# Optimization experiments

Hardware: AMD Instinct MI355X
Metric: run time of the kernel (lower is better)

## Reference

```python
import jax, jax.numpy as jnp
import numpy as np

B, S, V, E, H, XD, C = 64, 512, 32000, 512, 1024, 512, 1024


def setup_inputs() -> dict:
    key = jax.random.key(0)
    ks = jax.random.split(key, 20)
    s = 0.02
    inp = {
        "X": jax.random.randint(ks[0], (B, S), 0, V),
        "h0": jax.random.normal(ks[1], (B, H), jnp.float32),
        "embed": jax.random.normal(ks[2], (V, E), jnp.float32) * s,
        "Wzh": jax.random.normal(ks[3], (H, H), jnp.float32) * s,
        "bzh": jnp.zeros((H,), jnp.float32),
        "Wzx": jax.random.normal(ks[4], (H, E), jnp.float32) * s,
        "bzx": jnp.zeros((H,), jnp.float32),
        "Wrh": jax.random.normal(ks[5], (H, H), jnp.float32) * s,
        "brh": jnp.zeros((H,), jnp.float32),
        "Wrx": jax.random.normal(ks[6], (H, E), jnp.float32) * s,
        "brx": jnp.zeros((H,), jnp.float32),
        "Wuh": jax.random.normal(ks[7], (H, H), jnp.float32) * s,
        "buh": jnp.zeros((H,), jnp.float32),
        "Wux": jax.random.normal(ks[8], (H, E), jnp.float32) * s,
        "bux": jnp.zeros((H,), jnp.float32),
        "Wxh": jax.random.normal(ks[9], (XD, H), jnp.float32) * s,
        "bxh": jnp.zeros((XD,), jnp.float32),
        "Wc": jax.random.normal(ks[10], (C, XD), jnp.float32) * s,
        "bc": jnp.zeros((C,), jnp.float32),
    }
    return inp


def reference(X, h0, embed, Wzh, bzh, Wzx, bzx, Wrh, brh, Wrx, brx,
              Wuh, buh, Wux, bux, Wxh, bxh, Wc, bc):
    x_embed = embed[X]                    # [B,S,E]
    xs = jnp.transpose(x_embed, (1, 0, 2))  # [S,B,E] for scan

    def step(ht, xt):
        zt = jax.nn.sigmoid(ht @ Wzh.T + bzh + xt @ Wzx.T + bzx)
        rt = jax.nn.sigmoid(ht @ Wrh.T + brh + xt @ Wrx.T + brx)
        ht_cand = jnp.tanh((rt * ht) @ Wuh.T + buh + xt @ Wux.T + bux)
        ht_new = (1.0 - zt) * ht + zt * ht_cand
        yt = ht_new @ Wxh.T + bxh          # [B,XD]
        yprob = yt @ Wc.T + bc             # [B,C]
        return ht_new, yprob

    _, yprobs = jax.lax.scan(step, h0, xs)  # [S,B,C]
    return jnp.transpose(yprobs, (1, 0, 2))  # [B,S,C]
```

## Files before the change

### kernel.cpp

```cpp
#include <hip/hip_runtime.h>

#define DEV __device__ __forceinline__

using bf16x8 = __attribute__((ext_vector_type(8))) short;
using u16x4  = __attribute__((ext_vector_type(4))) unsigned short;
using f32x4  = __attribute__((ext_vector_type(4))) float;

constexpr int B_ = 64, S_ = 512, V_ = 32000, E_ = 512, H_ = 1024, C_ = 1024;
constexpr int NWG = 64;
constexpr int JS  = 16;

constexpr size_t OFF_FH    = 0;
constexpr size_t OFF_FR    = 1024;
constexpr size_t OFF_BIASG = 2048;
constexpr size_t OFF_BCOMB = OFF_BIASG + 3072*4;
constexpr size_t OFF_HB    = OFF_BCOMB + 1024*4;
constexpr size_t OFF_RHB   = OFF_HB + 131072;
constexpr size_t OFF_WCOMB = OFF_RHB + 131072;
constexpr size_t OFF_WXALL = OFF_WCOMB + (size_t)C_*H_*2;
constexpr size_t OFF_WZF   = OFF_WXALL + (size_t)3072*512*2;
constexpr size_t OFF_WRF   = OFF_WZF + (size_t)NWG*32768;
constexpr size_t OFF_WUF   = OFF_WRF + (size_t)NWG*32768;
constexpr size_t OFF_EMB   = OFF_WUF + (size_t)NWG*32768;
constexpr size_t OFF_G     = OFF_EMB + (size_t)V_*E_*2;
constexpr size_t OFF_HS    = OFF_G + (size_t)S_*B_*3072*2;
constexpr size_t WS_NEED   = OFF_HS + (size_t)S_*B_*H_*2;

DEV unsigned short f2bf(float f){
  unsigned int x; __builtin_memcpy(&x, &f, 4);
  x += 0x7fffu + ((x>>16)&1u);
  return (unsigned short)(x>>16);
}
DEV float bf2f(unsigned short u){
  unsigned int x = ((unsigned int)u)<<16; float f; __builtin_memcpy(&f,&x,4); return f;
}

DEV int4 ld16_coh(const char* p){
  int4 r;
  asm volatile("global_load_dwordx4 %0, %1, off sc0 sc1" : "=v"(r) : "v"(p) : "memory");
  return r;
}
DEV void st16_coh(char* p, bf16x8 v){
  asm volatile("global_store_dwordx4 %0, %1, off sc0 sc1" :: "v"(p), "v"(v) : "memory");
}
DEV uint2 ld8_plain(const char* p){
  uint2 r;
  asm volatile("global_load_dwordx2 %0, %1, off" : "=v"(r) : "v"(p) : "memory");
  return r;
}

#define WAITVM(N) do{ asm volatile("s_waitcnt vmcnt(" #N ")" ::: "memory"); \
                      __builtin_amdgcn_sched_barrier(0); }while(0)
#define WAITLGKM() do{ asm volatile("s_waitcnt lgkmcnt(0)" ::: "memory"); \
                       __builtin_amdgcn_sched_barrier(0); }while(0)

__global__ void k_cvt_embed(const float* __restrict__ src, unsigned short* __restrict__ dst){
  for (int i = blockIdx.x*blockDim.x + threadIdx.x; i < V_*E_; i += gridDim.x*blockDim.x)
    dst[i] = f2bf(src[i]);
}

__global__ void k_build_wx(const float* __restrict__ Wzx, const float* __restrict__ Wrx,
                           const float* __restrict__ Wux, unsigned short* __restrict__ out){
  for (int i = blockIdx.x*blockDim.x + threadIdx.x; i < 3072*512; i += gridDim.x*blockDim.x){
    int n = i>>9, k = i&511;
    int g = n>>10, r = n&1023;
    const float* W = (g==0) ? Wzx : (g==1) ? Wrx : Wux;
    out[i] = f2bf(W[(size_t)r*512 + k]);
  }
}

__global__ void k_biasg(const float* bzh, const float* bzx, const float* brh, const float* brx,
                        const float* buh, const float* bux, float* __restrict__ out){
  for (int i = blockIdx.x*blockDim.x + threadIdx.x; i < 3072; i += gridDim.x*blockDim.x){
    int g = i>>10, r = i&1023;
    float v = (g==0) ? (bzh[r]+bzx[r]) : (g==1) ? (brh[r]+brx[r]) : (buh[r]+bux[r]);
    out[i] = v;
  }
}

__global__ void k_fragW(const float* __restrict__ W, unsigned short* __restrict__ out){
  for (int i = blockIdx.x*blockDim.x + threadIdx.x; i < NWG*32*64*8; i += gridDim.x*blockDim.x){
    int e=i&7, l=(i>>3)&63, ck=(i>>9)&31, g=i>>14;
    out[i] = f2bf(W[(size_t)(g*JS+(l&15))*H_ + ck*32 + ((l>>4)<<3) + e]);
  }
}

__global__ __launch_bounds__(256) void k_wcomb(const float* __restrict__ Wc,
                                               const float* __restrict__ Wxh,
                                               unsigned short* __restrict__ Wcomb){
  __shared__ float wc[16][512];
  const int c0 = blockIdx.x*16;
  const int tid = threadIdx.x;
  for (int q = tid; q < 16*512; q += 256)
    wc[q>>9][q&511] = Wc[(size_t)(c0 + (q>>9))*512 + (q&511)];
  __syncthreads();
  const int h4 = tid*4;
  f32x4 acc[16];
  #pragma unroll
  for (int ci=0; ci<16; ++ci) acc[ci] = (f32x4){0.f,0.f,0.f,0.f};
  for (int x=0; x<512; ++x){
    f32x4 wv = *(const f32x4*)(Wxh + (size_t)x*H_ + h4);
    #pragma unroll
    for (int ci=0; ci<16; ++ci) acc[ci] += wc[ci][x] * wv;
  }
  #pragma unroll
  for (int ci=0; ci<16; ++ci)
    #pragma unroll
    for (int e=0; e<4; ++e)
      Wcomb[(size_t)(c0+ci)*H_ + h4 + e] = f2bf(acc[ci][e]);
}

__global__ void k_bcomb(const float* __restrict__ Wc, const float* __restrict__ bxh,
                        const float* __restrict__ bc, float* __restrict__ out){
  int c = blockIdx.x*blockDim.x + threadIdx.x;
  if (c >= C_) return;
  float s = bc[c];
  for (int x=0; x<512; ++x) s += Wc[(size_t)c*512 + x]*bxh[x];
  out[c] = s;
}

__global__ void k_hinit(const float* __restrict__ h0, unsigned short* __restrict__ hbF){
  int i = blockIdx.x*256 + threadIdx.x;
  int e=i&7, l=(i>>3)&63, ck=(i>>9)&31, q=i>>14;
  hbF[i] = f2bf(h0[(size_t)(q*16+(l&15))*H_ + ck*32 + ((l>>4)<<3) + e]);
}

template<bool GATHER, int MODE>
__global__ __launch_bounds__(256) void gemm_bt(
  const unsigned short* __restrict__ Asrc, const int* __restrict__ Xidx,
  const unsigned short* __restrict__ embB,
  const unsigned short* __restrict__ Bw, const float* __restrict__ bias,
  void* __restrict__ Cout, int K, int KT, int NTN, int ldc)
{
  __shared__ unsigned short ldsA[128*64];
  __shared__ unsigned short ldsB[128*64];
  const int bid = blockIdx.x;
  const int tm = bid / NTN, tn = bid % NTN;
  const int m0 = tm*128, n0 = tn*128;
  const int tid = threadIdx.x, wave = tid>>6, lane = tid&63;
  const int wm = (wave&1)*64, wn = (wave>>1)*64;

  const char* srcA[4]; const char* srcB[4];
  int rr[4], cc[4];
  #pragma unroll
  for (int s=0; s<4; ++s){
    int L = s*4096 + tid*16;
    int r = L>>7, cb = L&127;
    rr[s]=r; cc[s]=cb;
    if constexpr (GATHER){
      int m = m0 + r; int tt = m>>6, bb = m&63;
      srcA[s] = (const char*)(embB + (size_t)Xidx[bb*S_ + tt]*(size_t)K);
    } else {
      srcA[s] = (const char*)(Asrc + (size_t)(m0+r)*(size_t)K);
    }
    srcB[s] = (const char*)(Bw + (size_t)(n0+r)*(size_t)K);
  }

  f32x4 acc[4][4];
  #pragma unroll
  for (int a=0;a<4;a++)
    #pragma unroll
    for (int b=0;b<4;b++) acc[a][b] = (f32x4){0.f,0.f,0.f,0.f};

  int4 ra[4], rb[4];
  auto loadRegs = [&](int kt){
    #pragma unroll
    for (int s=0;s<4;s++){
      ra[s] = *(const int4*)(srcA[s] + (size_t)kt*128 + cc[s]);
      rb[s] = *(const int4*)(srcB[s] + (size_t)kt*128 + cc[s]);
    }
  };
  auto writeLDS = [&](){
    #pragma unroll
    for (int s=0;s<4;s++){
      int off = (rr[s]<<7) + (cc[s] ^ ((rr[s]&7)<<4));
      *(int4*)((char*)ldsA + off) = ra[s];
      *(int4*)((char*)ldsB + off) = rb[s];
    }
  };

  loadRegs(0);
  for (int kt=0; kt<KT; ++kt){
    __syncthreads();
    writeLDS();
    if (kt+1 < KT) loadRegs(kt+1);
    __syncthreads();
    #pragma unroll
    for (int ck=0; ck<2; ++ck){
      bf16x8 af[4], bfr[4];
      #pragma unroll
      for (int q=0;q<4;q++){
        int ar = wm + q*16 + (lane&15);
        int ao = (ar<<7) + (((ck<<6) + ((lane>>4)<<4)) ^ ((ar&7)<<4));
        af[q] = *(const bf16x8*)((const char*)ldsA + ao);
        int br = wn + q*16 + (lane&15);
        int bo = (br<<7) + (((ck<<6) + ((lane>>4)<<4)) ^ ((br&7)<<4));
        bfr[q] = *(const bf16x8*)((const char*)ldsB + bo);
      }
      #pragma unroll
      for (int mi=0;mi<4;mi++)
        #pragma unroll
        for (int ni=0;ni<4;ni++)
          acc[mi][ni] = __builtin_amdgcn_mfma_f32_16x16x32_bf16(af[mi], bfr[ni], acc[mi][ni], 0,0,0);
    }
  }

  #pragma unroll
  for (int mi=0;mi<4;mi++){
    #pragma unroll
    for (int ni=0;ni<4;ni++){
      int gm = m0 + wm + mi*16 + ((lane>>4)<<2);
      int gn = n0 + wn + ni*16 + (lane&15);
      float bv = bias[gn];
      if constexpr (MODE == 1){
        #pragma unroll
        for (int r2=0;r2<4;r2++){
          float v = acc[mi][ni][r2] + bv;
          int m = gm + r2;
          ((float*)Cout)[ (size_t)((m&63)*S_ + (m>>6))*(size_t)ldc + gn ] = v;
        }
      } else {
        int t0 = gm>>6, b0 = gm&63;
        u16x4 pk;
        #pragma unroll
        for (int r2=0;r2<4;r2++) pk[r2] = f2bf(acc[mi][ni][r2] + bv);
        *(u16x4*)((unsigned short*)Cout + ((size_t)t0*3072 + gn)*64 + b0) = pk;
      }
    }
  }
}

DEV void pollq(const unsigned int* f, unsigned int p, int lane, int bg){
  const unsigned int* a = f + lane*4 + bg;
  int guard = 0;
  for(;;){
    unsigned int v = __hip_atomic_load(a, __ATOMIC_RELAXED, __HIP_MEMORY_SCOPE_AGENT);
    if (__all((int)(v >= p))) break;
    __builtin_amdgcn_s_sleep(1);
    if (++guard > (1<<24)) break;
  }
}

__global__ __launch_bounds__(256,1) void k_scan(const float* __restrict__ h0, char* __restrict__ ws){
  const int wg = blockIdx.x;
  const int tid = threadIdx.x;
  const int bg = tid>>6, lane = tid&63;
  const int j0 = wg*JS;
  const int ckw = wg>>1, hw = wg&1;

  unsigned int* fH = (unsigned int*)(ws + OFF_FH);
  unsigned int* fR = (unsigned int*)(ws + OFF_FR);
  const unsigned short* G = (const unsigned short*)(ws + OFF_G);
  unsigned short* Hs  = (unsigned short*)(ws + OFF_HS);

  const char* EXH = ws + OFF_HB  + ((size_t)bg<<15);
  const char* EXR = ws + OFF_RHB + ((size_t)bg<<15);
  char* pubR = ws + OFF_RHB + ((size_t)bg<<15) + (ckw<<10) + (hw<<9);
  char* pubH = ws + OFF_HB  + ((size_t)bg<<15) + (ckw<<10) + (hw<<9);

  extern __shared__ char lds[];
  char* fz  = lds;
  char* frm = lds + 32768;
  char* fum = lds + 65536;
  unsigned short* tA = (unsigned short*)(lds + 98304  + bg*512);
  unsigned short* tB = (unsigned short*)(lds + 100352 + bg*512);

  {
    const int4* sz = (const int4*)(ws + OFF_WZF + ((size_t)wg<<15));
    const int4* sr = (const int4*)(ws + OFF_WRF + ((size_t)wg<<15));
    const int4* su = (const int4*)(ws + OFF_WUF + ((size_t)wg<<15));
    #pragma unroll
    for (int i=0;i<8;i++) ((int4*)fz )[tid + i*256] = sz[tid + i*256];
    #pragma unroll
    for (int i=0;i<8;i++) ((int4*)frm)[tid + i*256] = sr[tid + i*256];
    #pragma unroll
    for (int i=0;i<8;i++) ((int4*)fum)[tid + i*256] = su[tid + i*256];
  }
  __syncthreads();

  const int c   = lane & 15;
  const int hi2 = lane >> 4;
  const int rbase = (bg<<4) + (hi2<<2);
  const int gzc = j0 + c, grc = 1024 + j0 + c, guc = 2048 + j0 + c;

  float h_own[4];
  #pragma unroll
  for (int r2=0;r2<4;r2++)
    h_own[r2] = h0[(size_t)(rbase+r2)*H_ + j0 + c];

#define LOAD32(base) { _Pragma("unroll") \
  for (int i=0;i<32;i++) b[i] = ld16_coh((base) + ((i*64+lane)<<4)); }
#define S1G(g0) { _Pragma("unroll") \
  for (int i=0;i<8;i++){ int ck=(g0)*8+i; \
    bf16x8 av = __builtin_bit_cast(bf16x8, b[ck]); \
    bf16x8 wz = *(const bf16x8*)(fz  + ((ck*64+lane)<<4)); \
    bf16x8 wr = *(const bf16x8*)(frm + ((ck*64+lane)<<4)); \
    if (i&1){ az1=__builtin_amdgcn_mfma_f32_16x16x32_bf16(av,wz,az1,0,0,0); \
              ar1=__builtin_amdgcn_mfma_f32_16x16x32_bf16(av,wr,ar1,0,0,0);} \
    else    { az0=__builtin_amdgcn_mfma_f32_16x16x32_bf16(av,wz,az0,0,0,0); \
              ar0=__builtin_amdgcn_mfma_f32_16x16x32_bf16(av,wr,ar0,0,0,0);} } }
#define S2G(g0) { _Pragma("unroll") \
  for (int i=0;i<8;i++){ int ck=(g0)*8+i; \
    bf16x8 av = __builtin_bit_cast(bf16x8, b[ck]); \
    bf16x8 wu = *(const bf16x8*)(fum + ((ck*64+lane)<<4)); \
    if (i&1) au1=__builtin_amdgcn_mfma_f32_16x16x32_bf16(av,wu,au1,0,0,0); \
    else     au0=__builtin_amdgcn_mfma_f32_16x16x32_bf16(av,wu,au0,0,0,0); } }

  for (int t=0; t<S_; ++t){
    uint2 gv1 = ld8_plain((const char*)(G + ((size_t)t*3072 + gzc)*64 + rbase));
    uint2 gv2 = ld8_plain((const char*)(G + ((size_t)t*3072 + grc)*64 + rbase));
    uint2 gv3 = ld8_plain((const char*)(G + ((size_t)t*3072 + guc)*64 + rbase));

    if (t > 0) pollq(fH, (unsigned)t, lane, bg);

    f32x4 az0=(f32x4){0,0,0,0}, az1=(f32x4){0,0,0,0};
    f32x4 ar0=(f32x4){0,0,0,0}, ar1=(f32x4){0,0,0,0};
    int4 b[32];
    LOAD32(EXH);
    WAITVM(24); S1G(0);
    WAITVM(16); S1G(1);
    WAITVM(8);  S1G(2);
    WAITVM(0);  S1G(3);
    f32x4 zpre = az0+az1, rpre = ar0+ar1;

    float zval[4];
    {
      unsigned short gz4[4] = {(unsigned short)(gv1.x&0xffffu),(unsigned short)(gv1.x>>16),
                               (unsigned short)(gv1.y&0xffffu),(unsigned short)(gv1.y>>16)};
      unsigned short gr4[4] = {(unsigned short)(gv2.x&0xffffu),(unsigned short)(gv2.x>>16),
                               (unsigned short)(gv2.y&0xffffu),(unsigned short)(gv2.y>>16)};
      #pragma unroll
      for (int r2=0;r2<4;r2++){
        float z = 1.f/(1.f + __expf(-(zpre[r2] + bf2f(gz4[r2]))));
        float r = 1.f/(1.f + __expf(-(rpre[r2] + bf2f(gr4[r2]))));
        zval[r2] = z;
        tA[(hi2*4 + r2)*16 + c] = f2bf(r * h_own[r2]);
      }
    }
    WAITLGKM();
    if (lane < 32){
      bf16x8 v = *(const bf16x8*)(tA + (lane&15)*16 + ((lane>>4)<<3));
      st16_coh(pubR + (lane<<4), v);
    }
    WAITVM(0);
    if (lane == 0)
      __hip_atomic_store(&fR[wg*4+bg], (unsigned)(t+1), __ATOMIC_RELAXED, __HIP_MEMORY_SCOPE_AGENT);
    pollq(fR, (unsigned)(t+1), lane, bg);

    f32x4 au0=(f32x4){0,0,0,0}, au1=(f32x4){0,0,0,0};
    LOAD32(EXR);
    WAITVM(24); S2G(0);
    WAITVM(16); S2G(1);
    WAITVM(8);  S2G(2);
    WAITVM(0);  S2G(3);
    f32x4 upre = au0+au1;

    {
      unsigned short gu4[4] = {(unsigned short)(gv3.x&0xffffu),(unsigned short)(gv3.x>>16),
                               (unsigned short)(gv3.y&0xffffu),(unsigned short)(gv3.y>>16)};
      #pragma unroll
      for (int r2=0;r2<4;r2++){
        float up = upre[r2] + bf2f(gu4[r2]);
        float e  = __expf(-2.f*up);
        float u  = (1.f - e)/(1.f + e);
        float hn = h_own[r2] + zval[r2]*(u - h_own[r2]);
        h_own[r2] = hn;
        tB[(hi2*4 + r2)*16 + c] = f2bf(hn);
      }
    }
    WAITLGKM();
    if (lane < 32){
      bf16x8 v = *(const bf16x8*)(tB + (lane&15)*16 + ((lane>>4)<<3));
      st16_coh(pubH + (lane<<4), v);
      *(bf16x8*)(Hs + (size_t)((t<<6) + (bg<<4) + (lane&15))*H_ + j0 + ((lane>>4)<<3)) = v;
    }
    WAITVM(0);
    if (lane == 0)
      __hip_atomic_store(&fH[wg*4+bg], (unsigned)(t+1), __ATOMIC_RELAXED, __HIP_MEMORY_SCOPE_AGENT);
  }
#undef LOAD32
#undef S1G
#undef S2G
}

extern "C" void kernel_launch(void* const* d_in, const int* in_sizes, int n_in,
                              void* d_out, int out_size, void* d_ws, size_t ws_size,
                              hipStream_t stream)
{
  const int*   X    = (const int*)  d_in[0];
  const float* h0   = (const float*)d_in[1];
  const float* emb  = (const float*)d_in[2];
  const float* Wzh  = (const float*)d_in[3];
  const float* bzh  = (const float*)d_in[4];
  const float* Wzx  = (const float*)d_in[5];
  const float* bzx  = (const float*)d_in[6];
  const float* Wrh  = (const float*)d_in[7];
  const float* brh  = (const float*)d_in[8];
  const float* Wrx  = (const float*)d_in[9];
  const float* brx  = (const float*)d_in[10];
  const float* Wuh  = (const float*)d_in[11];
  const float* buh  = (const float*)d_in[12];
  const float* Wux  = (const float*)d_in[13];
  const float* bux  = (const float*)d_in[14];
  const float* Wxh  = (const float*)d_in[15];
  const float* bxh  = (const float*)d_in[16];
  const float* Wc   = (const float*)d_in[17];
  const float* bc   = (const float*)d_in[18];
  (void)in_sizes; (void)n_in;

  char* ws = (char*)d_ws;
  if (ws_size < WS_NEED){
    hipMemsetAsync(d_out, 0, (size_t)out_size*4, stream);
    return;
  }

  hipMemsetAsync(ws + OFF_FH, 0, 2048, stream);

  k_cvt_embed<<<4096, 256, 0, stream>>>(emb, (unsigned short*)(ws + OFF_EMB));
  k_build_wx <<<1536, 256, 0, stream>>>(Wzx, Wrx, Wux, (unsigned short*)(ws + OFF_WXALL));
  k_biasg    <<<12,   256, 0, stream>>>(bzh, bzx, brh, brx, buh, bux, (float*)(ws + OFF_BIASG));
  k_fragW    <<<2048, 256, 0, stream>>>(Wzh, (unsigned short*)(ws + OFF_WZF));
  k_fragW    <<<2048, 256, 0, stream>>>(Wrh, (unsigned short*)(ws + OFF_WRF));
  k_fragW    <<<2048, 256, 0, stream>>>(Wuh, (unsigned short*)(ws + OFF_WUF));
  k_wcomb    <<<64,   256, 0, stream>>>(Wc, Wxh, (unsigned short*)(ws + OFF_WCOMB));
  k_bcomb    <<<4,    256, 0, stream>>>(Wc, bxh, bc, (float*)(ws + OFF_BCOMB));
  k_hinit    <<<256,  256, 0, stream>>>(h0, (unsigned short*)(ws + OFF_HB));

  gemm_bt<true,2><<<6144, 256, 0, stream>>>(
      nullptr, X, (const unsigned short*)(ws + OFF_EMB),
      (const unsigned short*)(ws + OFF_WXALL), (const float*)(ws + OFF_BIASG),
      (void*)(ws + OFF_G), 512, 8, 24, 3072);

  hipFuncSetAttribute((const void*)k_scan, hipFuncAttributeMaxDynamicSharedMemorySize, 102400);
  k_scan<<<NWG, 256, 102400, stream>>>(h0, ws);

  gemm_bt<false,1><<<2048, 256, 0, stream>>>(
      (const unsigned short*)(ws + OFF_HS), nullptr, nullptr,
      (const unsigned short*)(ws + OFF_WCOMB), (const float*)(ws + OFF_BCOMB),
      d_out, 1024, 16, 8, 1024);
}
```

Measured before the change: 7.692 ms.

## Split scan barrier into per-group polls overlapped with chunked loads

Replaces the full all-workgroup flag poll before each matmul phase with four group-wise polls, one per 16 producer workgroups. After each poll, the loads for that chunk of h or r*h are issued and consumed with double buffering, and the group order is rotated per workgroup. The aim is to start loading and computing on data from producers that are already done instead of waiting on the slowest of all 64. It adds more polling loop iterations and smaller load batches, which could add latency if all producers finish at about the same time.

```diff
diff --git a/kernel.cpp b/kernel.cpp
--- a/kernel.cpp
+++ b/kernel.cpp
@@ -230,8 +230,8 @@
   }
 }
 
-DEV void pollq(const unsigned int* f, unsigned int p, int lane, int bg){
-  const unsigned int* a = f + lane*4 + bg;
+DEV void pollgrp(const unsigned int* f, unsigned int p, int lane, int bg, int g){
+  const unsigned int* a = f + ((unsigned)(g*16 + (lane&15))*4 + bg);
   int guard = 0;
   for(;;){
     unsigned int v = __hip_atomic_load(a, __ATOMIC_RELAXED, __HIP_MEMORY_SCOPE_AGENT);
@@ -283,25 +283,27 @@
   const int rbase = (bg<<4) + (hi2<<2);
   const int gzc = j0 + c, grc = 1024 + j0 + c, guc = 2048 + j0 + c;
 
+  const int gA=(wg)&3, gB=(wg+1)&3, gC=(wg+2)&3, gD=(wg+3)&3;
+
   float h_own[4];
   #pragma unroll
   for (int r2=0;r2<4;r2++)
     h_own[r2] = h0[(size_t)(rbase+r2)*H_ + j0 + c];
 
-#define LOAD32(base) { _Pragma("unroll") \
-  for (int i=0;i<32;i++) b[i] = ld16_coh((base) + ((i*64+lane)<<4)); }
-#define S1G(g0) { _Pragma("unroll") \
-  for (int i=0;i<8;i++){ int ck=(g0)*8+i; \
-    bf16x8 av = __builtin_bit_cast(bf16x8, b[ck]); \
+#define ISSUE8(buf, base, g) { _Pragma("unroll") \
+  for (int i=0;i<8;i++) buf[i] = ld16_coh((base) + ((((g)*8+i)*64+lane)<<4)); }
+#define CONS1(buf, g) { _Pragma("unroll") \
+  for (int i=0;i<8;i++){ int ck=(g)*8+i; \
+    bf16x8 av = __builtin_bit_cast(bf16x8, buf[i]); \
     bf16x8 wz = *(const bf16x8*)(fz  + ((ck*64+lane)<<4)); \
     bf16x8 wr = *(const bf16x8*)(frm + ((ck*64+lane)<<4)); \
     if (i&1){ az1=__builtin_amdgcn_mfma_f32_16x16x32_bf16(av,wz,az1,0,0,0); \
               ar1=__builtin_amdgcn_mfma_f32_16x16x32_bf16(av,wr,ar1,0,0,0);} \
     else    { az0=__builtin_amdgcn_mfma_f32_16x16x32_bf16(av,wz,az0,0,0,0); \
               ar0=__builtin_amdgcn_mfma_f32_16x16x32_bf16(av,wr,ar0,0,0,0);} } }
-#define S2G(g0) { _Pragma("unroll") \
-  for (int i=0;i<8;i++){ int ck=(g0)*8+i; \
-    bf16x8 av = __builtin_bit_cast(bf16x8, b[ck]); \
+#define CONS2(buf, g) { _Pragma("unroll") \
+  for (int i=0;i<8;i++){ int ck=(g)*8+i; \
+    bf16x8 av = __builtin_bit_cast(bf16x8, buf[i]); \
     bf16x8 wu = *(const bf16x8*)(fum + ((ck*64+lane)<<4)); \
     if (i&1) au1=__builtin_amdgcn_mfma_f32_16x16x32_bf16(av,wu,au1,0,0,0); \
     else     au0=__builtin_amdgcn_mfma_f32_16x16x32_bf16(av,wu,au0,0,0,0); } }
@@ -311,16 +313,23 @@
     uint2 gv2 = ld8_plain((const char*)(G + ((size_t)t*3072 + grc)*64 + rbase));
     uint2 gv3 = ld8_plain((const char*)(G + ((size_t)t*3072 + guc)*64 + rbase));
 
-    if (t > 0) pollq(fH, (unsigned)t, lane, bg);
-
     f32x4 az0=(f32x4){0,0,0,0}, az1=(f32x4){0,0,0,0};
     f32x4 ar0=(f32x4){0,0,0,0}, ar1=(f32x4){0,0,0,0};
-    int4 b[32];
-    LOAD32(EXH);
-    WAITVM(24); S1G(0);
-    WAITVM(16); S1G(1);
-    WAITVM(8);  S1G(2);
-    WAITVM(0);  S1G(3);
+    {
+      int4 bA[8], bB[8];
+      if (t>0) pollgrp(fH, (unsigned)t, lane, bg, gA);
+      ISSUE8(bA, EXH, gA);
+      if (t>0) pollgrp(fH, (unsigned)t, lane, bg, gB);
+      ISSUE8(bB, EXH, gB);
+      WAITVM(8);  CONS1(bA, gA);
+      if (t>0) pollgrp(fH, (unsigned)t, lane, bg, gC);
+      ISSUE8(bA, EXH, gC);
+      WAITVM(8);  CONS1(bB, gB);
+      if (t>0) pollgrp(fH, (unsigned)t, lane, bg, gD);
+      ISSUE8(bB, EXH, gD);
+      WAITVM(8);  CONS1(bA, gC);
+      WAITVM(0);  CONS1(bB, gD);
+    }
     f32x4 zpre = az0+az1, rpre = ar0+ar1;
 
     float zval[4];
@@ -345,14 +354,23 @@
     WAITVM(0);
     if (lane == 0)
       __hip_atomic_store(&fR[wg*4+bg], (unsigned)(t+1), __ATOMIC_RELAXED, __HIP_MEMORY_SCOPE_AGENT);
-    pollq(fR, (unsigned)(t+1), lane, bg);
 
     f32x4 au0=(f32x4){0,0,0,0}, au1=(f32x4){0,0,0,0};
-    LOAD32(EXR);
-    WAITVM(24); S2G(0);
-    WAITVM(16); S2G(1);
-    WAITVM(8);  S2G(2);
-    WAITVM(0);  S2G(3);
+    {
+      int4 bA[8], bB[8];
+      pollgrp(fR, (unsigned)(t+1), lane, bg, gA);
+      ISSUE8(bA, EXR, gA);
+      pollgrp(fR, (unsigned)(t+1), lane, bg, gB);
+      ISSUE8(bB, EXR, gB);
+      WAITVM(8);  CONS2(bA, gA);
+      pollgrp(fR, (unsigned)(t+1), lane, bg, gC);
+      ISSUE8(bA, EXR, gC);
+      WAITVM(8);  CONS2(bB, gB);
+      pollgrp(fR, (unsigned)(t+1), lane, bg, gD);
+      ISSUE8(bB, EXR, gD);
+      WAITVM(8);  CONS2(bA, gC);
+      WAITVM(0);  CONS2(bB, gD);
+    }
     f32x4 upre = au0+au1;
 
     {
@@ -378,9 +396,9 @@
     if (lane == 0)
       __hip_atomic_store(&fH[wg*4+bg], (unsigned)(t+1), __ATOMIC_RELAXED, __HIP_MEMORY_SCOPE_AGENT);
   }
-#undef LOAD32
-#undef S1G
-#undef S2G
+#undef ISSUE8
+#undef CONS1
+#undef CONS2
 }
 
 extern "C" void kernel_launch(void* const* d_in, const int* in_sizes, int n_in,
@@ -410,11 +428,11 @@
 
   char* ws = (char*)d_ws;
   if (ws_size < WS_NEED){
-    hipMemsetAsync(d_out, 0, (size_t)out_size*4, stream);
+    (void)hipMemsetAsync(d_out, 0, (size_t)out_size*4, stream);
     return;
   }
 
-  hipMemsetAsync(ws + OFF_FH, 0, 2048, stream);
+  (void)hipMemsetAsync(ws + OFF_FH, 0, 2048, stream);
 
   k_cvt_embed<<<4096, 256, 0, stream>>>(emb, (unsigned short*)(ws + OFF_EMB));
   k_build_wx <<<1536, 256, 0, stream>>>(Wzx, Wrx, Wux, (unsigned short*)(ws + OFF_WXALL));
@@ -431,7 +449,7 @@
       (const unsigned short*)(ws + OFF_WXALL), (const float*)(ws + OFF_BIASG),
       (void*)(ws + OFF_G), 512, 8, 24, 3072);
 
-  hipFuncSetAttribute((const void*)k_scan, hipFuncAttributeMaxDynamicSharedMemorySize, 102400);
+  (void)hipFuncSetAttribute((const void*)k_scan, hipFuncAttributeMaxDynamicSharedMemorySize, 102400);
   k_scan<<<NWG, 256, 102400, stream>>>(h0, ws);
 
   gemm_bt<false,1><<<2048, 256, 0, stream>>>(
```

Result: faster. 6.809 ms (-11.5%).
